# Performance work log

Measured on AMD Instinct MI355X. Metric: run time of the kernel, lower is better.

Reference implementation:

```python
import jax, jax.numpy as jnp
import numpy as np


def setup_inputs() -> dict:
    key = jax.random.key(0)
    ks = jax.random.split(key, 7)
    B, Q, K, D, H = 4, 256, 1024, 512, 128
    return {
        "queries": jax.random.normal(ks[0], (B, Q, D), dtype=jnp.float32),
        "keys": jax.random.normal(ks[1], (B, K, D), dtype=jnp.float32),
        "values": jax.random.normal(ks[2], (B, K, D), dtype=jnp.float32),
        "Wq": jax.random.normal(ks[3], (D, H), dtype=jnp.float32) * (1.0 / np.sqrt(D)),
        "Wk": jax.random.normal(ks[4], (D, H), dtype=jnp.float32) * (1.0 / np.sqrt(D)),
        "wv": jax.random.normal(ks[5], (H,), dtype=jnp.float32) * (1.0 / np.sqrt(H)),
        "valid_lens": jax.random.randint(ks[6], (B,), 1, K + 1, dtype=jnp.int32),
    }


def reference(queries, keys, values, Wq, Wk, wv, valid_lens):
    # queries: (B,Q,D), keys/values: (B,K,D)
    q = jnp.einsum("bqd,dh->bqh", queries, Wq)
    k = jnp.einsum("bkd,dh->bkh", keys, Wk)
    # broadcast-add -> (B,Q,K,H), tanh, project with wv -> scores (B,Q,K)
    features = jnp.tanh(q[:, :, None, :] + k[:, None, :, :])
    scores = jnp.einsum("bqkh,h->bqk", features, wv)
    # masked softmax: original replaces masked logits with 0 (not -inf)
    K_len = keys.shape[1]
    mask = jnp.arange(K_len)[None, None, :] < valid_lens[:, None, None]  # (B,1,K)
    masked = jnp.where(mask, scores, 0.0)
    attn = jax.nn.softmax(masked, axis=-1)
    # dropout is identity at inference
    return jnp.einsum("bqk,bkd->bqd", attn, values)
```

## Files before the change

kernel.cpp:

```cpp
#include <hip/hip_runtime.h>

#define NB 4
#define NQ 256
#define NK 1024
#define ND 512
#define NH 128

typedef _Float16 half8_t __attribute__((ext_vector_type(8)));
typedef _Float16 half4_t __attribute__((ext_vector_type(4)));
typedef float f32x4_t __attribute__((ext_vector_type(4)));

#define TANH_C 2.8853900817779268f

__global__ __launch_bounds__(256) void prep_kernel(
    const float* __restrict__ Wq, const float* __restrict__ Wk,
    const float* __restrict__ values, _Float16* __restrict__ WQT,
    _Float16* __restrict__ WKT, _Float16* __restrict__ vT,
    float4* __restrict__ out4) {
  __shared__ float smem[64 * 130];
  const int bid = blockIdx.x;
  const int t = threadIdx.x;

  if (bid < 16) {
    float(*tile)[129] = (float(*)[129])smem;
    const float* W = (bid >= 8) ? Wk : Wq;
    _Float16* WT = (bid >= 8) ? WKT : WQT;
    const int d0 = (bid & 7) * 64;
    #pragma unroll
    for (int j = 0; j < 32; ++j) {
      const int idx = t + j * 256;
      tile[idx >> 7][idx & 127] = W[(size_t)(d0 + (idx >> 7)) * NH + (idx & 127)];
    }
    __syncthreads();
    #pragma unroll
    for (int j = 0; j < 32; ++j) {
      const int idx = t + j * 256;
      const int h = idx >> 6, r = idx & 63;
      WT[(size_t)h * ND + d0 + r] = (_Float16)tile[r][h];
    }
    return;
  }

  const int vb = bid - 16;
  out4[(size_t)vb * 256 + t] = make_float4(0.f, 0.f, 0.f, 0.f);

  float(*tile)[65] = (float(*)[65])smem;
  const int dt = vb & 7;
  const int kt = (vb >> 3) & 15;
  const int b = vb >> 7;
  const int k0 = kt * 64, d0 = dt * 64;
  {
    const int kl = t >> 4, dl4 = (t & 15) * 4;
    #pragma unroll
    for (int i = 0; i < 4; ++i) {
      const float4 v = *(const float4*)(
          values + ((size_t)(b * NK + k0 + kl + i * 16)) * ND + d0 + dl4);
      tile[dl4 + 0][kl + i * 16] = v.x;
      tile[dl4 + 1][kl + i * 16] = v.y;
      tile[dl4 + 2][kl + i * 16] = v.z;
      tile[dl4 + 3][kl + i * 16] = v.w;
    }
  }
  __syncthreads();
  const int dr = t >> 2, kc = (t & 3) * 16;
  half8_t h0, h1;
  #pragma unroll
  for (int ii = 0; ii < 8; ++ii) {
    h0[ii] = (_Float16)tile[dr][kc + ii];
    h1[ii] = (_Float16)tile[dr][kc + 8 + ii];
  }
  _Float16* dst = vT + ((size_t)(b * ND + d0 + dr)) * NK + k0 + kc;
  *(half8_t*)dst = h0;
  *(half8_t*)(dst + 8) = h1;
}

__global__ __launch_bounds__(256) void proj_mfma_kernel(
    const float* __restrict__ queries, const float* __restrict__ keys,
    const _Float16* __restrict__ WQT, const _Float16* __restrict__ WKT,
    float* __restrict__ EQ, float* __restrict__ EKT) {
  const int bid = blockIdx.x;
  const int row0 = bid * 16;
  const bool is_q = row0 < NB * NQ;
  const float* X = is_q ? queries : (keys - (size_t)NB * NQ * ND);
  const _Float16* WT = is_q ? WQT : WKT;

  const int w = threadIdx.x >> 6;
  const int l = threadIdx.x & 63;
  const int h0 = w * 32;

  const float* xrow = X + (size_t)(row0 + (l & 15)) * ND + (l >> 4) * 8;
  const _Float16* wt0 = WT + (size_t)(h0 + (l & 15)) * ND + (l >> 4) * 8;
  const _Float16* wt1 = wt0 + 16 * ND;

  f32x4_t acc0 = {0.f, 0.f, 0.f, 0.f};
  f32x4_t acc1 = {0.f, 0.f, 0.f, 0.f};
  #pragma unroll 4
  for (int d = 0; d < ND; d += 32) {
    const float4 x0 = *(const float4*)(xrow + d);
    const float4 x1 = *(const float4*)(xrow + d + 4);
    half8_t a;
    a[0] = (_Float16)x0.x; a[1] = (_Float16)x0.y;
    a[2] = (_Float16)x0.z; a[3] = (_Float16)x0.w;
    a[4] = (_Float16)x1.x; a[5] = (_Float16)x1.y;
    a[6] = (_Float16)x1.z; a[7] = (_Float16)x1.w;
    const half8_t b0 = *(const half8_t*)(wt0 + d);
    const half8_t b1 = *(const half8_t*)(wt1 + d);
    acc0 = __builtin_amdgcn_mfma_f32_16x16x32_f16(a, b0, acc0, 0, 0, 0);
    acc1 = __builtin_amdgcn_mfma_f32_16x16x32_f16(a, b1, acc1, 0, 0, 0);
  }
  const int mrow = row0 + (l >> 4) * 4;
  const int hcol = h0 + (l & 15);
  if (is_q) {
    #pragma unroll
    for (int r = 0; r < 4; ++r) {
      EQ[(size_t)(mrow + r) * NH + hcol] = __builtin_exp2f(TANH_C * acc0[r]);
      EQ[(size_t)(mrow + r) * NH + hcol + 16] = __builtin_exp2f(TANH_C * acc1[r]);
    }
  } else {
    const int rowk = mrow - NB * NQ;
    const int bb = rowk >> 10;
    const int kk = rowk & 1023;
    float4 v0, v1;
    v0.x = __builtin_exp2f(TANH_C * acc0[0]);
    v0.y = __builtin_exp2f(TANH_C * acc0[1]);
    v0.z = __builtin_exp2f(TANH_C * acc0[2]);
    v0.w = __builtin_exp2f(TANH_C * acc0[3]);
    v1.x = __builtin_exp2f(TANH_C * acc1[0]);
    v1.y = __builtin_exp2f(TANH_C * acc1[1]);
    v1.z = __builtin_exp2f(TANH_C * acc1[2]);
    v1.w = __builtin_exp2f(TANH_C * acc1[3]);
    *(float4*)(EKT + ((size_t)(bb * NH + hcol)) * NK + kk) = v0;
    *(float4*)(EKT + ((size_t)(bb * NH + hcol + 16)) * NK + kk) = v1;
  }
}

__global__ __launch_bounds__(512, 4) void scores_softmax_kernel(
    const float* __restrict__ EQ, const float* __restrict__ EKT,
    const float* __restrict__ wv, const int* __restrict__ vlen,
    _Float16* __restrict__ attn_h) {
  __shared__ float4 eqwv2[2][64];
  __shared__ float red[2][2][4];
  const int bid = blockIdx.x;
  const int b = bid >> 7;
  const int q0 = (bid & 127) * 2;
  const int t = threadIdx.x;
  const int w = t >> 6;
  const int myq = w & 1;
  const int kc = w >> 1;
  const int l = t & 63;
  const int vl = vlen[b];

  if (t < 128) {
    const int qq = t >> 6, i = t & 63;
    const float* eqrow = EQ + (size_t)(b * NQ + q0 + qq) * NH;
    eqwv2[qq][i] = make_float4(eqrow[2 * i], wv[2 * i],
                               eqrow[2 * i + 1], wv[2 * i + 1]);
  }
  __syncthreads();

  float Wsum;
  {
    const float4 a = eqwv2[0][l];
    Wsum = a.y + a.w;
    #pragma unroll
    for (int off = 32; off; off >>= 1) Wsum += __shfl_xor(Wsum, off);
  }

  const int k0 = kc * 256;
  float acc0 = 0.f, acc1 = 0.f, acc2 = 0.f, acc3 = 0.f;
  if (k0 < vl) {
    const float* ekb = EKT + (size_t)(b * NH) * NK + k0 + l * 4;
    #pragma unroll 4
    for (int hh = 0; hh < 64; ++hh) {
      const float4 q4 = eqwv2[myq][hh];
      const float4 ea = *(const float4*)(ekb + (size_t)(2 * hh) * NK);
      const float4 eb = *(const float4*)(ekb + (size_t)(2 * hh + 1) * NK);
      {
        const float da = fmaf(q4.x, ea.x, 1.f), db = fmaf(q4.z, eb.x, 1.f);
        acc0 = fmaf(fmaf(q4.y, db, q4.w * da),
                    __builtin_amdgcn_rcpf(da * db), acc0);
      }
      {
        const float da = fmaf(q4.x, ea.y, 1.f), db = fmaf(q4.z, eb.y, 1.f);
        acc1 = fmaf(fmaf(q4.y, db, q4.w * da),
                    __builtin_amdgcn_rcpf(da * db), acc1);
      }
      {
        const float da = fmaf(q4.x, ea.z, 1.f), db = fmaf(q4.z, eb.z, 1.f);
        acc2 = fmaf(fmaf(q4.y, db, q4.w * da),
                    __builtin_amdgcn_rcpf(da * db), acc2);
      }
      {
        const float da = fmaf(q4.x, ea.w, 1.f), db = fmaf(q4.z, eb.w, 1.f);
        acc3 = fmaf(fmaf(q4.y, db, q4.w * da),
                    __builtin_amdgcn_rcpf(da * db), acc3);
      }
    }
  }

  const int kbase = k0 + l * 4;
  float s0 = (kbase + 0 < vl) ? (Wsum - 2.f * acc0) : 0.f;
  float s1 = (kbase + 1 < vl) ? (Wsum - 2.f * acc1) : 0.f;
  float s2 = (kbase + 2 < vl) ? (Wsum - 2.f * acc2) : 0.f;
  float s3 = (kbase + 3 < vl) ? (Wsum - 2.f * acc3) : 0.f;

  float m = fmaxf(fmaxf(s0, s1), fmaxf(s2, s3));
  #pragma unroll
  for (int off = 32; off; off >>= 1) m = fmaxf(m, __shfl_xor(m, off));
  if (l == 0) red[0][myq][kc] = m;
  __syncthreads();
  m = fmaxf(fmaxf(red[0][myq][0], red[0][myq][1]),
            fmaxf(red[0][myq][2], red[0][myq][3]));
  const float ce = 1.4426950408889634f;
  s0 = __builtin_exp2f(ce * (s0 - m));
  s1 = __builtin_exp2f(ce * (s1 - m));
  s2 = __builtin_exp2f(ce * (s2 - m));
  s3 = __builtin_exp2f(ce * (s3 - m));
  float sum = s0 + s1 + s2 + s3;
  #pragma unroll
  for (int off = 32; off; off >>= 1) sum += __shfl_xor(sum, off);
  if (l == 0) red[1][myq][kc] = sum;
  __syncthreads();
  const float Z =
      red[1][myq][0] + red[1][myq][1] + red[1][myq][2] + red[1][myq][3];
  const float inv = 1.0f / Z;
  half4_t h;
  h[0] = (_Float16)(s0 * inv);
  h[1] = (_Float16)(s1 * inv);
  h[2] = (_Float16)(s2 * inv);
  h[3] = (_Float16)(s3 * inv);
  *(half4_t*)(attn_h + (size_t)(b * NQ + q0 + myq) * NK + kbase) = h;
}

__global__ __launch_bounds__(256) void pv_mfma_kernel(
    const _Float16* __restrict__ attn_h, const _Float16* __restrict__ vT,
    float* __restrict__ out) {
  const int bid = blockIdx.x;
  const int kc  = bid & 3;
  const int nt8 = (bid >> 2) & 7;
  const int mt  = (bid >> 5) & 7;
  const int b   = bid >> 8;
  const int w = threadIdx.x >> 6;
  const int l = threadIdx.x & 63;
  const int mtile = w & 1;
  const int ntile0 = (w >> 1) * 2;
  const int q_lo = mt * 32 + mtile * 16;
  const int d_lo = nt8 * 64 + ntile0 * 16;
  const int k0 = kc * 256;

  const _Float16* arow =
      attn_h + ((size_t)(b * NQ + q_lo + (l & 15))) * NK + k0 + (l >> 4) * 8;
  const _Float16* brow0 =
      vT + ((size_t)(b * ND + d_lo + (l & 15))) * NK + k0 + (l >> 4) * 8;
  const _Float16* brow1 = brow0 + 16 * NK;

  f32x4_t acc0 = {0.f, 0.f, 0.f, 0.f};
  f32x4_t acc1 = {0.f, 0.f, 0.f, 0.f};
  #pragma unroll
  for (int ks = 0; ks < 256; ks += 32) {
    const half8_t a  = *(const half8_t*)(arow + ks);
    const half8_t b0 = *(const half8_t*)(brow0 + ks);
    const half8_t b1 = *(const half8_t*)(brow1 + ks);
    acc0 = __builtin_amdgcn_mfma_f32_16x16x32_f16(a, b0, acc0, 0, 0, 0);
    acc1 = __builtin_amdgcn_mfma_f32_16x16x32_f16(a, b1, acc1, 0, 0, 0);
  }
  const int mrow = q_lo + (l >> 4) * 4;
  const int dcol = d_lo + (l & 15);
  #pragma unroll
  for (int r = 0; r < 4; ++r) {
    atomicAdd(&out[(size_t)(b * NQ + mrow + r) * ND + dcol], acc0[r]);
    atomicAdd(&out[(size_t)(b * NQ + mrow + r) * ND + dcol + 16], acc1[r]);
  }
}

extern "C" void kernel_launch(void* const* d_in, const int* in_sizes, int n_in,
                              void* d_out, int out_size, void* d_ws, size_t ws_size,
                              hipStream_t stream) {
  const float* queries = (const float*)d_in[0];
  const float* keys    = (const float*)d_in[1];
  const float* values  = (const float*)d_in[2];
  const float* Wq      = (const float*)d_in[3];
  const float* Wk      = (const float*)d_in[4];
  const float* wv      = (const float*)d_in[5];
  const int*   vlen    = (const int*)d_in[6];
  float* out = (float*)d_out;

  char* ws = (char*)d_ws;
  float*     EQ     = (float*)(ws);
  float*     EKT    = (float*)(ws + (512 << 10));
  _Float16*  attn_h = (_Float16*)(ws + (2560 << 10));
  _Float16*  vT     = (_Float16*)(ws + (4608 << 10));
  _Float16*  WQT    = (_Float16*)(ws + (8704 << 10));
  _Float16*  WKT    = (_Float16*)(ws + (8832 << 10));

  prep_kernel<<<528, 256, 0, stream>>>(Wq, Wk, values, WQT, WKT, vT,
                                       (float4*)out);
  proj_mfma_kernel<<<(NB * NQ + NB * NK) / 16, 256, 0, stream>>>(
      queries, keys, WQT, WKT, EQ, EKT);
  scores_softmax_kernel<<<NB * (NQ / 2), 512, 0, stream>>>(EQ, EKT, wv, vlen,
                                                           attn_h);
  pv_mfma_kernel<<<NB * 8 * 8 * 4, 256, 0, stream>>>(attn_h, vT, out);
}
```

Before: 59.23 us.

## Drop split-K atomics in PV and share EKT loads across two queries

The PV kernel now walks the full K=1024 reduction per block with one 16x16 MFMA tile per wave and writes the output directly. This removes the atomicAdd accumulation and the output zeroing in prep_kernel. The scores kernel now has each wave handle both queries over a 128-key chunk, so each EKT load is reused for two queries and the reductions span 8 waves. The trade-offs are fewer PV blocks (512) with a longer serial MFMA chain, and narrower float2 loads in the scores kernel.

```diff
diff --git a/kernel.cpp b/kernel.cpp
--- a/kernel.cpp
+++ b/kernel.cpp
@@ -8,6 +8,7 @@
 
 typedef _Float16 half8_t __attribute__((ext_vector_type(8)));
 typedef _Float16 half4_t __attribute__((ext_vector_type(4)));
+typedef _Float16 half2_t __attribute__((ext_vector_type(2)));
 typedef float f32x4_t __attribute__((ext_vector_type(4)));
 
 #define TANH_C 2.8853900817779268f
@@ -15,8 +16,7 @@
 __global__ __launch_bounds__(256) void prep_kernel(
     const float* __restrict__ Wq, const float* __restrict__ Wk,
     const float* __restrict__ values, _Float16* __restrict__ WQT,
-    _Float16* __restrict__ WKT, _Float16* __restrict__ vT,
-    float4* __restrict__ out4) {
+    _Float16* __restrict__ WKT, _Float16* __restrict__ vT) {
   __shared__ float smem[64 * 130];
   const int bid = blockIdx.x;
   const int t = threadIdx.x;
@@ -42,8 +42,6 @@
   }
 
   const int vb = bid - 16;
-  out4[(size_t)vb * 256 + t] = make_float4(0.f, 0.f, 0.f, 0.f);
-
   float(*tile)[65] = (float(*)[65])smem;
   const int dt = vb & 7;
   const int kt = (vb >> 3) & 15;
@@ -139,14 +137,12 @@
     const float* __restrict__ wv, const int* __restrict__ vlen,
     _Float16* __restrict__ attn_h) {
   __shared__ float4 eqwv2[2][64];
-  __shared__ float red[2][2][4];
+  __shared__ float red[2][2][8];
   const int bid = blockIdx.x;
   const int b = bid >> 7;
   const int q0 = (bid & 127) * 2;
   const int t = threadIdx.x;
   const int w = t >> 6;
-  const int myq = w & 1;
-  const int kc = w >> 1;
   const int l = t & 63;
   const int vl = vlen[b];
 
@@ -166,111 +162,112 @@
     for (int off = 32; off; off >>= 1) Wsum += __shfl_xor(Wsum, off);
   }
 
-  const int k0 = kc * 256;
-  float acc0 = 0.f, acc1 = 0.f, acc2 = 0.f, acc3 = 0.f;
+  const int k0 = w * 128;
+  float a00 = 0.f, a01 = 0.f, a10 = 0.f, a11 = 0.f;
   if (k0 < vl) {
-    const float* ekb = EKT + (size_t)(b * NH) * NK + k0 + l * 4;
+    const float* ekb = EKT + (size_t)(b * NH) * NK + k0 + l * 2;
     #pragma unroll 4
     for (int hh = 0; hh < 64; ++hh) {
-      const float4 q4 = eqwv2[myq][hh];
-      const float4 ea = *(const float4*)(ekb + (size_t)(2 * hh) * NK);
-      const float4 eb = *(const float4*)(ekb + (size_t)(2 * hh + 1) * NK);
-      {
-        const float da = fmaf(q4.x, ea.x, 1.f), db = fmaf(q4.z, eb.x, 1.f);
-        acc0 = fmaf(fmaf(q4.y, db, q4.w * da),
-                    __builtin_amdgcn_rcpf(da * db), acc0);
-      }
-      {
-        const float da = fmaf(q4.x, ea.y, 1.f), db = fmaf(q4.z, eb.y, 1.f);
-        acc1 = fmaf(fmaf(q4.y, db, q4.w * da),
-                    __builtin_amdgcn_rcpf(da * db), acc1);
-      }
-      {
-        const float da = fmaf(q4.x, ea.z, 1.f), db = fmaf(q4.z, eb.z, 1.f);
-        acc2 = fmaf(fmaf(q4.y, db, q4.w * da),
-                    __builtin_amdgcn_rcpf(da * db), acc2);
-      }
-      {
-        const float da = fmaf(q4.x, ea.w, 1.f), db = fmaf(q4.z, eb.w, 1.f);
-        acc3 = fmaf(fmaf(q4.y, db, q4.w * da),
-                    __builtin_amdgcn_rcpf(da * db), acc3);
-      }
-    }
-  }
-
-  const int kbase = k0 + l * 4;
-  float s0 = (kbase + 0 < vl) ? (Wsum - 2.f * acc0) : 0.f;
-  float s1 = (kbase + 1 < vl) ? (Wsum - 2.f * acc1) : 0.f;
-  float s2 = (kbase + 2 < vl) ? (Wsum - 2.f * acc2) : 0.f;
-  float s3 = (kbase + 3 < vl) ? (Wsum - 2.f * acc3) : 0.f;
-
-  float m = fmaxf(fmaxf(s0, s1), fmaxf(s2, s3));
-  #pragma unroll
-  for (int off = 32; off; off >>= 1) m = fmaxf(m, __shfl_xor(m, off));
-  if (l == 0) red[0][myq][kc] = m;
-  __syncthreads();
-  m = fmaxf(fmaxf(red[0][myq][0], red[0][myq][1]),
-            fmaxf(red[0][myq][2], red[0][myq][3]));
+      const float4 qw0 = eqwv2[0][hh];
+      const float4 qw1 = eqwv2[1][hh];
+      const float2 ea = *(const float2*)(ekb + (size_t)(2 * hh) * NK);
+      const float2 eb = *(const float2*)(ekb + (size_t)(2 * hh + 1) * NK);
+      {
+        const float da = fmaf(qw0.x, ea.x, 1.f), db = fmaf(qw0.z, eb.x, 1.f);
+        a00 = fmaf(fmaf(qw0.y, db, qw0.w * da),
+                   __builtin_amdgcn_rcpf(da * db), a00);
+      }
+      {
+        const float da = fmaf(qw0.x, ea.y, 1.f), db = fmaf(qw0.z, eb.y, 1.f);
+        a01 = fmaf(fmaf(qw0.y, db, qw0.w * da),
+                   __builtin_amdgcn_rcpf(da * db), a01);
+      }
+      {
+        const float da = fmaf(qw1.x, ea.x, 1.f), db = fmaf(qw1.z, eb.x, 1.f);
+        a10 = fmaf(fmaf(qw1.y, db, qw1.w * da),
+                   __builtin_amdgcn_rcpf(da * db), a10);
+      }
+      {
+        const float da = fmaf(qw1.x, ea.y, 1.f), db = fmaf(qw1.z, eb.y, 1.f);
+        a11 = fmaf(fmaf(qw1.y, db, qw1.w * da),
+                   __builtin_amdgcn_rcpf(da * db), a11);
+      }
+    }
+  }
+
+  const int kA = k0 + l * 2, kB = kA + 1;
+  float s00 = (kA < vl) ? (Wsum - 2.f * a00) : 0.f;
+  float s01 = (kB < vl) ? (Wsum - 2.f * a01) : 0.f;
+  float s10 = (kA < vl) ? (Wsum - 2.f * a10) : 0.f;
+  float s11 = (kB < vl) ? (Wsum - 2.f * a11) : 0.f;
+
+  float m0 = fmaxf(s00, s01), m1 = fmaxf(s10, s11);
+  #pragma unroll
+  for (int off = 32; off; off >>= 1) {
+    m0 = fmaxf(m0, __shfl_xor(m0, off));
+    m1 = fmaxf(m1, __shfl_xor(m1, off));
+  }
+  if (l == 0) { red[0][0][w] = m0; red[0][1][w] = m1; }
+  __syncthreads();
+  m0 = red[0][0][0]; m1 = red[0][1][0];
+  #pragma unroll
+  for (int i = 1; i < 8; ++i) {
+    m0 = fmaxf(m0, red[0][0][i]);
+    m1 = fmaxf(m1, red[0][1][i]);
+  }
   const float ce = 1.4426950408889634f;
-  s0 = __builtin_exp2f(ce * (s0 - m));
-  s1 = __builtin_exp2f(ce * (s1 - m));
-  s2 = __builtin_exp2f(ce * (s2 - m));
-  s3 = __builtin_exp2f(ce * (s3 - m));
-  float sum = s0 + s1 + s2 + s3;
-  #pragma unroll
-  for (int off = 32; off; off >>= 1) sum += __shfl_xor(sum, off);
-  if (l == 0) red[1][myq][kc] = sum;
-  __syncthreads();
-  const float Z =
-      red[1][myq][0] + red[1][myq][1] + red[1][myq][2] + red[1][myq][3];
-  const float inv = 1.0f / Z;
-  half4_t h;
-  h[0] = (_Float16)(s0 * inv);
-  h[1] = (_Float16)(s1 * inv);
-  h[2] = (_Float16)(s2 * inv);
-  h[3] = (_Float16)(s3 * inv);
-  *(half4_t*)(attn_h + (size_t)(b * NQ + q0 + myq) * NK + kbase) = h;
+  s00 = __builtin_exp2f(ce * (s00 - m0));
+  s01 = __builtin_exp2f(ce * (s01 - m0));
+  s10 = __builtin_exp2f(ce * (s10 - m1));
+  s11 = __builtin_exp2f(ce * (s11 - m1));
+  float sum0 = s00 + s01, sum1 = s10 + s11;
+  #pragma unroll
+  for (int off = 32; off; off >>= 1) {
+    sum0 += __shfl_xor(sum0, off);
+    sum1 += __shfl_xor(sum1, off);
+  }
+  if (l == 0) { red[1][0][w] = sum0; red[1][1][w] = sum1; }
+  __syncthreads();
+  float Z0 = 0.f, Z1 = 0.f;
+  #pragma unroll
+  for (int i = 0; i < 8; ++i) { Z0 += red[1][0][i]; Z1 += red[1][1][i]; }
+  const float inv0 = 1.0f / Z0, inv1 = 1.0f / Z1;
+  half2_t h0, h1;
+  h0[0] = (_Float16)(s00 * inv0); h0[1] = (_Float16)(s01 * inv0);
+  h1[0] = (_Float16)(s10 * inv1); h1[1] = (_Float16)(s11 * inv1);
+  *(half2_t*)(attn_h + (size_t)(b * NQ + q0) * NK + kA) = h0;
+  *(half2_t*)(attn_h + (size_t)(b * NQ + q0 + 1) * NK + kA) = h1;
 }
 
 __global__ __launch_bounds__(256) void pv_mfma_kernel(
     const _Float16* __restrict__ attn_h, const _Float16* __restrict__ vT,
     float* __restrict__ out) {
   const int bid = blockIdx.x;
-  const int kc  = bid & 3;
-  const int nt8 = (bid >> 2) & 7;
-  const int mt  = (bid >> 5) & 7;
-  const int b   = bid >> 8;
+  const int dt = bid & 7;
+  const int qt = (bid >> 3) & 15;
+  const int b  = bid >> 7;
   const int w = threadIdx.x >> 6;
   const int l = threadIdx.x & 63;
-  const int mtile = w & 1;
-  const int ntile0 = (w >> 1) * 2;
-  const int q_lo = mt * 32 + mtile * 16;
-  const int d_lo = nt8 * 64 + ntile0 * 16;
-  const int k0 = kc * 256;
+  const int q_lo = qt * 16;
+  const int d_lo = dt * 64 + w * 16;
 
   const _Float16* arow =
-      attn_h + ((size_t)(b * NQ + q_lo + (l & 15))) * NK + k0 + (l >> 4) * 8;
-  const _Float16* brow0 =
-      vT + ((size_t)(b * ND + d_lo + (l & 15))) * NK + k0 + (l >> 4) * 8;
-  const _Float16* brow1 = brow0 + 16 * NK;
-
-  f32x4_t acc0 = {0.f, 0.f, 0.f, 0.f};
-  f32x4_t acc1 = {0.f, 0.f, 0.f, 0.f};
-  #pragma unroll
-  for (int ks = 0; ks < 256; ks += 32) {
-    const half8_t a  = *(const half8_t*)(arow + ks);
-    const half8_t b0 = *(const half8_t*)(brow0 + ks);
-    const half8_t b1 = *(const half8_t*)(brow1 + ks);
-    acc0 = __builtin_amdgcn_mfma_f32_16x16x32_f16(a, b0, acc0, 0, 0, 0);
-    acc1 = __builtin_amdgcn_mfma_f32_16x16x32_f16(a, b1, acc1, 0, 0, 0);
+      attn_h + ((size_t)(b * NQ + q_lo + (l & 15))) * NK + (l >> 4) * 8;
+  const _Float16* brow =
+      vT + ((size_t)(b * ND + d_lo + (l & 15))) * NK + (l >> 4) * 8;
+
+  f32x4_t acc = {0.f, 0.f, 0.f, 0.f};
+  #pragma unroll 8
+  for (int ks = 0; ks < NK; ks += 32) {
+    const half8_t a = *(const half8_t*)(arow + ks);
+    const half8_t bb = *(const half8_t*)(brow + ks);
+    acc = __builtin_amdgcn_mfma_f32_16x16x32_f16(a, bb, acc, 0, 0, 0);
   }
   const int mrow = q_lo + (l >> 4) * 4;
   const int dcol = d_lo + (l & 15);
   #pragma unroll
-  for (int r = 0; r < 4; ++r) {
-    atomicAdd(&out[(size_t)(b * NQ + mrow + r) * ND + dcol], acc0[r]);
-    atomicAdd(&out[(size_t)(b * NQ + mrow + r) * ND + dcol + 16], acc1[r]);
-  }
+  for (int r = 0; r < 4; ++r)
+    out[(size_t)(b * NQ + mrow + r) * ND + dcol] = acc[r];
 }
 
 extern "C" void kernel_launch(void* const* d_in, const int* in_sizes, int n_in,
@@ -293,11 +290,10 @@
   _Float16*  WQT    = (_Float16*)(ws + (8704 << 10));
   _Float16*  WKT    = (_Float16*)(ws + (8832 << 10));
 
-  prep_kernel<<<528, 256, 0, stream>>>(Wq, Wk, values, WQT, WKT, vT,
-                                       (float4*)out);
+  prep_kernel<<<528, 256, 0, stream>>>(Wq, Wk, values, WQT, WKT, vT);
   proj_mfma_kernel<<<(NB * NQ + NB * NK) / 16, 256, 0, stream>>>(
       queries, keys, WQT, WKT, EQ, EKT);
   scores_softmax_kernel<<<NB * (NQ / 2), 512, 0, stream>>>(EQ, EKT, wv, vlen,
                                                            attn_h);
-  pv_mfma_kernel<<<NB * 8 * 8 * 4, 256, 0, stream>>>(attn_h, vT, out);
-}
+  pv_mfma_kernel<<<NB * 16 * 8, 256, 0, stream>>>(attn_h, vT, out);
+}
```

New measurement: 58.40 us. Within noise of the previous version (-1.4%).
